# Kernel tuning notes

Hardware: AMD Instinct MI355X
Metric: run time of the kernel (lower is better)

Reference implementation:

```python
import jax, jax.numpy as jnp
import numpy as np

NHEAD = 8
LAYER_NAMES = ('self', 'cross', 'self', 'cross')
EPS = 1e-6


def ln(x, g, b, eps=1e-5):
    m = jnp.mean(x, -1, keepdims=True)
    v = jnp.mean((x - m) ** 2, -1, keepdims=True)
    return (x - m) * jax.lax.rsqrt(v + eps) * g + b


def linear_attention(q, k, v, q_mask, kv_mask):
    # q: [N, L, H, D], k/v: [N, S, H, D]; LoFTR LinearAttention (elu+1 feature map)
    Q = jax.nn.elu(q) + 1.0
    K = jax.nn.elu(k) + 1.0
    if q_mask is not None:
        Q = Q * q_mask[:, :, None, None].astype(Q.dtype)
    if kv_mask is not None:
        mk = kv_mask[:, :, None, None].astype(K.dtype)
        K = K * mk
        v = v * mk
    v_len = v.shape[1]
    v = v / v_len
    KV = jnp.einsum('nshd,nshv->nhdv', K, v)
    Z = 1.0 / (jnp.einsum('nlhd,nhd->nlh', Q, K.sum(1)) + EPS)
    return jnp.einsum('nlhd,nhdv,nlh->nlhv', Q, KV, Z) * v_len


def enc_layer(x, src, q_mask, kv_mask, Wq, Wk, Wv, Wm, W1, W2, g1, b1, g2, b2):
    # x: [N, L, C], src: [N, S, C]
    N, L, C = x.shape
    S = src.shape[1]
    H, D = NHEAD, C // NHEAD
    q = (x @ Wq).reshape(N, L, H, D)
    k = (src @ Wk).reshape(N, S, H, D)
    v = (src @ Wv).reshape(N, S, H, D)
    msg = linear_attention(q, k, v, q_mask, kv_mask).reshape(N, L, C)
    msg = ln(msg @ Wm, g1, b1)
    msg = ln(jnp.tanh(jnp.concatenate([x, msg], axis=-1) @ W1) @ W2, g2, b2)
    return x + msg


def sample_descriptors(kp, fmap, s):
    # kp: [B, L, K, 2] (x, y) raw-image pixel coords; fmap: [B, C, H, W]; s: stride
    B, C, H, W = fmap.shape
    k = kp - s / 2 + 0.5
    denom = jnp.array([W * s - s / 2 - 0.5, H * s - s / 2 - 0.5], dtype=kp.dtype)
    k = (k / denom) * 2.0 - 1.0  # normalized [-1, 1]
    px = (k[..., 0] + 1.0) * 0.5 * (W - 1)  # align_corners=True grid_sample
    py = (k[..., 1] + 1.0) * 0.5 * (H - 1)
    x0 = jnp.floor(px)
    y0 = jnp.floor(py)
    wx = (px - x0)[..., None]
    wy = (py - y0)[..., None]
    x0i = jnp.clip(x0, 0, W - 1).astype(jnp.int32)
    x1i = jnp.clip(x0 + 1, 0, W - 1).astype(jnp.int32)
    y0i = jnp.clip(y0, 0, H - 1).astype(jnp.int32)
    y1i = jnp.clip(y0 + 1, 0, H - 1).astype(jnp.int32)
    fm = jnp.transpose(fmap, (0, 2, 3, 1))  # [B, H, W, C]
    bidx = jnp.arange(B)[:, None, None]
    g00 = fm[bidx, y0i, x0i]
    g01 = fm[bidx, y0i, x1i]
    g10 = fm[bidx, y1i, x0i]
    g11 = fm[bidx, y1i, x1i]
    out = (1 - wy) * ((1 - wx) * g00 + wx * g01) + wy * ((1 - wx) * g10 + wx * g11)
    # SuperPoint-style L2 normalization of sampled descriptors
    out = out / (jnp.linalg.norm(out, axis=-1, keepdims=True) + 1e-8)
    return out  # [B, L, K, C]


def geo_transformer(feat0, feat1, kp0_cross, kp1_cross, mask_self0, mask_self1,
                    mask_cross0, mask_cross1, Wq, Wk, Wv, Wm, W1, W2, g1, b1, g2, b2,
                    h0, w0, h1, w1, scale):
    B, L0, C = feat0.shape
    L1 = feat1.shape[1]
    K = kp0_cross.shape[2]
    for i, name in enumerate(LAYER_NAMES):
        p = (Wq[i], Wk[i], Wv[i], Wm[i], W1[i], W2[i], g1[i], b1[i], g2[i], b2[i])
        if name == 'self':
            # source = masked subset of x == full source with kv-mask (v_length cancels)
            feat0 = enc_layer(feat0, feat0, None, mask_self0, *p)
            feat1 = enc_layer(feat1, feat1, None, mask_self1, *p)
        else:
            fmap0 = jnp.transpose(feat0.reshape(B, h0, w0, C), (0, 3, 1, 2))
            fmap1 = jnp.transpose(feat1.reshape(B, h1, w1, C), (0, 3, 1, 2))
            f0c = sample_descriptors(kp0_cross, fmap0, scale)  # [B, L1, K, C]
            f1c = sample_descriptors(kp1_cross, fmap1, scale)  # [B, L0, K, C]
            x0 = feat0.reshape(B * L0, 1, C)
            x1 = feat1.reshape(B * L1, 1, C)
            nf0 = enc_layer(x0, f1c.reshape(B * L0, K, C), None,
                            mask_cross1.reshape(B * L0, K), *p)
            nf1 = enc_layer(x1, f0c.reshape(B * L1, K, C), None,
                            mask_cross0.reshape(B * L1, K), *p)
            feat0 = nf0.reshape(B, L0, C)
            feat1 = nf1.reshape(B, L1, C)
    return feat0, feat1


def setup_inputs() -> dict:
    key = jax.random.key(0)
    B, H0, W0, C, K, S, NL = 2, 64, 64, 256, 9, 8, 4
    L = H0 * W0
    ks = jax.random.split(key, 16)
    std = (2.0 / (C + C)) ** 0.5
    std2 = (2.0 / (2 * C + 2 * C)) ** 0.5
    std3 = (2.0 / (2 * C + C)) ** 0.5
    kp0 = jnp.stack([
        jax.random.uniform(ks[2], (B, L, K)) * (W0 * S),
        jax.random.uniform(ks[3], (B, L, K)) * (H0 * S)], axis=-1)
    kp1 = jnp.stack([
        jax.random.uniform(ks[4], (B, L, K)) * (W0 * S),
        jax.random.uniform(ks[5], (B, L, K)) * (H0 * S)], axis=-1)
    return {
        'feat0': jax.random.normal(ks[0], (B, L, C), jnp.float32),
        'feat1': jax.random.normal(ks[1], (B, L, C), jnp.float32),
        'kp0_cross': kp0.astype(jnp.float32),
        'kp1_cross': kp1.astype(jnp.float32),
        'mask_self0': jax.random.bernoulli(ks[6], 0.9, (B, L)),
        'mask_self1': jax.random.bernoulli(ks[7], 0.9, (B, L)),
        'mask_cross0': jax.random.bernoulli(ks[8], 0.8, (B, L, K)),
        'mask_cross1': jax.random.bernoulli(ks[9], 0.8, (B, L, K)),
        'Wq': jax.random.normal(ks[10], (NL, C, C), jnp.float32) * std,
        'Wk': jax.random.normal(ks[11], (NL, C, C), jnp.float32) * std,
        'Wv': jax.random.normal(ks[12], (NL, C, C), jnp.float32) * std,
        'Wm': jax.random.normal(ks[13], (NL, C, C), jnp.float32) * std,
        'W1': jax.random.normal(ks[14], (NL, 2 * C, 2 * C), jnp.float32) * std2,
        'W2': jax.random.normal(ks[15], (NL, 2 * C, C), jnp.float32) * std3,
        'g1': jnp.ones((NL, C), jnp.float32),
        'b1': jnp.zeros((NL, C), jnp.float32),
        'g2': jnp.ones((NL, C), jnp.float32),
        'b2': jnp.zeros((NL, C), jnp.float32),
        'h0': H0, 'w0': W0, 'h1': H0, 'w1': W0, 'scale': S,
    }


def reference(feat0, feat1, kp0_cross, kp1_cross, mask_self0, mask_self1,
              mask_cross0, mask_cross1, Wq, Wk, Wv, Wm, W1, W2, g1, b1, g2, b2,
              h0, w0, h1, w1, scale):
    return geo_transformer(feat0, feat1, kp0_cross, kp1_cross, mask_self0, mask_self1,
                           mask_cross0, mask_cross1, Wq, Wk, Wv, Wm, W1, W2,
                           g1, b1, g2, b2, h0, w0, h1, w1, scale)
```

## Files before the change

### kernel.cpp

```cpp
#include <hip/hip_runtime.h>
#include <cstddef>


#define NROWS 16384

typedef unsigned short ushort_t;
typedef __attribute__((ext_vector_type(8))) short short8;
typedef __attribute__((ext_vector_type(4))) float f32x4;
typedef __attribute__((ext_vector_type(4))) unsigned short ushort4_t;
typedef __attribute__((ext_vector_type(8))) unsigned short ushort8_t;

__device__ __forceinline__ float b2f(unsigned short u) {
    union { unsigned int i; float f; } v; v.i = (unsigned int)u << 16; return v.f;
}
__device__ __forceinline__ unsigned short f2b(float x) {
    union { float f; unsigned int i; } v; v.f = x;
    unsigned int r = v.i + 0x7fffu + ((v.i >> 16) & 1u);
    return (unsigned short)(r >> 16);
}
__device__ __forceinline__ float elu1(float x) {
    return x > 0.f ? x + 1.f : __expf(x);
}

#define ASYNC_COPY16(gptr, lptr) \
    __builtin_amdgcn_global_load_lds((const __attribute__((address_space(1))) void*)(gptr), \
                                     (__attribute__((address_space(3))) void*)(lptr), 16, 0, 0)

template<int ACT>
__global__ __launch_bounds__(256) void gemm_bf16_kernel(
    const ushort_t* __restrict__ A0, const ushort_t* __restrict__ A1, int ksplit,
    int lda0, int lda1, const ushort_t* __restrict__ Wt, int ldw,
    ushort_t* __restrict__ C, int ldc, int Kd)
{
    __shared__ ushort_t As[128 * 32];
    __shared__ ushort_t Bs[128 * 32];

    int tid = threadIdx.x;
    int m0 = blockIdx.y * 128;
    int n0 = blockIdx.x * 128;
    int lane = tid & 63, w = tid >> 6;
    int wrow = w >> 1, wcol = w & 1;
    int quad = lane >> 4, l16 = lane & 15;

    f32x4 acc[4][4];
    #pragma unroll
    for (int i = 0; i < 4; i++)
        #pragma unroll
        for (int j = 0; j < 4; j++) acc[i][j] = (f32x4){0.f, 0.f, 0.f, 0.f};

    int c0 = tid, c1 = tid + 256;
    int ar0 = c0 >> 2, ac0 = (c0 & 3) * 8;
    int ar1 = c1 >> 2, ac1 = (c1 & 3) * 8;

    for (int kb = 0; kb < Kd; kb += 32) {
        const ushort_t* Ab; int lda, kc;
        if (kb < ksplit) { Ab = A0; lda = lda0; kc = kb; }
        else             { Ab = A1; lda = lda1; kc = kb - ksplit; }

        ASYNC_COPY16(Ab + (size_t)(m0 + ar0) * lda + kc + ac0, (char*)As + c0 * 16);
        ASYNC_COPY16(Ab + (size_t)(m0 + ar1) * lda + kc + ac1, (char*)As + c1 * 16);
        ASYNC_COPY16(Wt + (size_t)(n0 + ar0) * ldw + kb + ac0, (char*)Bs + c0 * 16);
        ASYNC_COPY16(Wt + (size_t)(n0 + ar1) * ldw + kb + ac1, (char*)Bs + c1 * 16);
        __syncthreads();

        short8 af[4], bf[4];
        #pragma unroll
        for (int mt = 0; mt < 4; mt++)
            af[mt] = *(const short8*)&As[(wrow * 64 + mt * 16 + l16) * 32 + quad * 8];
        #pragma unroll
        for (int nt = 0; nt < 4; nt++)
            bf[nt] = *(const short8*)&Bs[(wcol * 64 + nt * 16 + l16) * 32 + quad * 8];
        #pragma unroll
        for (int mt = 0; mt < 4; mt++)
            #pragma unroll
            for (int nt = 0; nt < 4; nt++)
                acc[mt][nt] = __builtin_amdgcn_mfma_f32_16x16x32_bf16(
                    af[mt], bf[nt], acc[mt][nt], 0, 0, 0);
        __syncthreads();
    }

    #pragma unroll
    for (int mt = 0; mt < 4; mt++) {
        int row = m0 + wrow * 64 + mt * 16 + quad * 4;
        #pragma unroll
        for (int nt = 0; nt < 4; nt++) {
            int col = n0 + wcol * 64 + nt * 16 + l16;
            #pragma unroll
            for (int r = 0; r < 4; r++) {
                float v = acc[mt][nt][r];
                if (ACT) v = tanhf(v);
                C[(size_t)(row + r) * ldc + col] = f2b(v);
            }
        }
    }
}

template<int RES>
__global__ __launch_bounds__(256) void gemm_ln_kernel(
    const ushort_t* __restrict__ A, int lda,
    const ushort_t* __restrict__ Wt, int ldw, int Kd,
    const float* __restrict__ g, const float* __restrict__ bp,
    ushort_t* __restrict__ OutBf,
    const float* __restrict__ Xin, float* __restrict__ Xout)
{
    __shared__ ushort_t As[64 * 64];
    __shared__ ushort_t Bs[256 * 64];
    __shared__ float rsum[4][64];
    __shared__ float rsq[4][64];

    int tid = threadIdx.x;
    int m0 = blockIdx.x * 64;
    int lane = tid & 63, w = tid >> 6;
    int quad = lane >> 4, l16 = lane & 15;

    f32x4 acc[4][4];
    #pragma unroll
    for (int i = 0; i < 4; i++)
        #pragma unroll
        for (int j = 0; j < 4; j++) acc[i][j] = (f32x4){0.f, 0.f, 0.f, 0.f};

    for (int kb = 0; kb < Kd; kb += 64) {
        #pragma unroll
        for (int q = 0; q < 2; q++) {
            int c = q * 256 + tid;
            ASYNC_COPY16(A + (size_t)(m0 + (c >> 3)) * lda + kb + (c & 7) * 8,
                         (char*)As + c * 16);
        }
        #pragma unroll
        for (int q = 0; q < 8; q++) {
            int c = q * 256 + tid;
            ASYNC_COPY16(Wt + (size_t)(c >> 3) * ldw + kb + (c & 7) * 8,
                         (char*)Bs + c * 16);
        }
        __syncthreads();

        #pragma unroll
        for (int kk = 0; kk < 2; kk++) {
            short8 af[4], bf[4];
            #pragma unroll
            for (int mt = 0; mt < 4; mt++)
                af[mt] = *(const short8*)&As[(mt * 16 + l16) * 64 + kk * 32 + quad * 8];
            #pragma unroll
            for (int nt = 0; nt < 4; nt++)
                bf[nt] = *(const short8*)&Bs[(w * 64 + nt * 16 + l16) * 64 + kk * 32 + quad * 8];
            #pragma unroll
            for (int mt = 0; mt < 4; mt++)
                #pragma unroll
                for (int nt = 0; nt < 4; nt++)
                    acc[mt][nt] = __builtin_amdgcn_mfma_f32_16x16x32_bf16(
                        af[mt], bf[nt], acc[mt][nt], 0, 0, 0);
        }
        __syncthreads();
    }

    float s1[4][4], s2[4][4];
    #pragma unroll
    for (int mt = 0; mt < 4; mt++)
        #pragma unroll
        for (int r = 0; r < 4; r++) {
            float s = 0.f, q = 0.f;
            #pragma unroll
            for (int nt = 0; nt < 4; nt++) {
                float v = acc[mt][nt][r];
                s += v; q += v * v;
            }
            #pragma unroll
            for (int off = 1; off < 16; off <<= 1) {
                s += __shfl_xor(s, off, 64);
                q += __shfl_xor(q, off, 64);
            }
            s1[mt][r] = s; s2[mt][r] = q;
        }
    if (l16 == 0) {
        #pragma unroll
        for (int mt = 0; mt < 4; mt++)
            #pragma unroll
            for (int r = 0; r < 4; r++) {
                rsum[w][mt * 16 + quad * 4 + r] = s1[mt][r];
                rsq[w][mt * 16 + quad * 4 + r]  = s2[mt][r];
            }
    }
    __syncthreads();

    #pragma unroll
    for (int mt = 0; mt < 4; mt++) {
        #pragma unroll
        for (int r = 0; r < 4; r++) {
            int rl = mt * 16 + quad * 4 + r;
            float s = rsum[0][rl] + rsum[1][rl] + rsum[2][rl] + rsum[3][rl];
            float q = rsq[0][rl] + rsq[1][rl] + rsq[2][rl] + rsq[3][rl];
            float m = s * (1.f / 256.f);
            float var = q * (1.f / 256.f) - m * m;
            float rs = rsqrtf(var + 1e-5f);
            size_t row = (size_t)(m0 + rl);
            #pragma unroll
            for (int nt = 0; nt < 4; nt++) {
                int col = w * 64 + nt * 16 + l16;
                float y = (acc[mt][nt][r] - m) * rs * g[col] + bp[col];
                if (RES) {
                    float xn = Xin[row * 256 + col] + y;
                    Xout[row * 256 + col] = xn;
                    OutBf[row * 256 + col] = f2b(xn);
                } else {
                    OutBf[row * 256 + col] = f2b(y);
                }
            }
        }
    }
}

__global__ __launch_bounds__(256) void wprep_kernel(
    const float* __restrict__ Wq, const float* __restrict__ Wk,
    const float* __restrict__ Wv, const float* __restrict__ Wm,
    const float* __restrict__ W1, const float* __restrict__ W2,
    ushort_t* __restrict__ Wqkvt, ushort_t* __restrict__ Wmt,
    ushort_t* __restrict__ W1t, ushort_t* __restrict__ W2t)
{
    int t = blockIdx.x;
    int layer = t / 640, r = t % 640;
    const float* src; ushort_t* dst;
    int ldsrc, lddst, tn, tk;
    if (r < 192) {
        int grp = r / 64, rr = r % 64; tn = rr / 8; tk = rr % 8;
        src = (grp == 0 ? Wq : grp == 1 ? Wk : Wv) + (size_t)layer * 65536;
        ldsrc = 256;
        dst = Wqkvt + (size_t)layer * 196608 + (size_t)grp * 65536;
        lddst = 256;
    } else if (r < 256) {
        int rr = r - 192; tn = rr / 8; tk = rr % 8;
        src = Wm + (size_t)layer * 65536; ldsrc = 256;
        dst = Wmt + (size_t)layer * 65536; lddst = 256;
    } else if (r < 512) {
        int rr = r - 256; tn = rr / 16; tk = rr % 16;
        src = W1 + (size_t)layer * 262144; ldsrc = 512;
        dst = W1t + (size_t)layer * 262144; lddst = 512;
    } else {
        int rr = r - 512; tn = rr / 16; tk = rr % 16;
        src = W2 + (size_t)layer * 131072; ldsrc = 256;
        dst = W2t + (size_t)layer * 131072; lddst = 512;
    }
    int n0 = tn * 32, k0 = tk * 32;
    __shared__ float tileS[32][33];
    int j = threadIdx.x & 31, i0 = threadIdx.x >> 5;
    #pragma unroll
    for (int p = 0; p < 4; p++) {
        int i = i0 + p * 8;
        tileS[i][j] = src[(size_t)(k0 + i) * ldsrc + n0 + j];
    }
    __syncthreads();
    #pragma unroll
    for (int p = 0; p < 4; p++) {
        int i = i0 + p * 8;
        dst[(size_t)(n0 + i) * lddst + k0 + j] = f2b(tileS[j][i]);
    }
}

__global__ __launch_bounds__(256) void init_kernel(
    const float* __restrict__ f0, const float* __restrict__ f1,
    float* __restrict__ X, ushort_t* __restrict__ Xbf)
{
    int idx = blockIdx.x * 256 + threadIdx.x;
    size_t e = (size_t)idx * 4;
    float4 v = (e < 2097152) ? *(const float4*)&f0[e] : *(const float4*)&f1[e - 2097152];
    *(float4*)&X[e] = v;
    ushort4_t u = { f2b(v.x), f2b(v.y), f2b(v.z), f2b(v.w) };
    *(ushort4_t*)&Xbf[e] = u;
}

__global__ __launch_bounds__(256) void kv_reduce_kernel(
    const ushort_t* __restrict__ QKV,
    const int* __restrict__ mask0, const int* __restrict__ mask1,
    float* __restrict__ KV, float* __restrict__ Ksum)
{
    int g = blockIdx.y;
    int t = g >> 4, b = (g >> 3) & 1, h = g & 7;
    const int* mask = t ? mask1 : mask0;
    int rowbase = t * 8192 + b * 4096;
    int s_begin = blockIdx.x * 256;

    __shared__ float sK[32][32];
    __shared__ float sV[32][32];

    int tid = threadIdx.x;
    int e  = tid & 31;
    int dq = tid >> 5;

    float acc[4] = {0.f, 0.f, 0.f, 0.f};
    float ks[4]  = {0.f, 0.f, 0.f, 0.f};

    for (int s0 = s_begin; s0 < s_begin + 256; s0 += 32) {
        #pragma unroll
        for (int q = 0; q < 2; q++) {
            int idx = tid + q * 256;
            int rl = idx >> 4;
            int part = idx & 15;
            int s = s0 + rl;
            size_t row = (size_t)(rowbase + s);
            float m = mask[b * 4096 + s] ? 1.f : 0.f;
            if (part < 8) {
                ushort4_t u = *(const ushort4_t*)&QKV[row * 768 + 256 + h * 32 + part * 4];
                float4 f = { elu1(b2f(u.x)) * m, elu1(b2f(u.y)) * m,
                             elu1(b2f(u.z)) * m, elu1(b2f(u.w)) * m };
                *(float4*)&sK[rl][part * 4] = f;
            } else {
                ushort4_t u = *(const ushort4_t*)&QKV[row * 768 + 512 + h * 32 + (part - 8) * 4];
                float4 f = { b2f(u.x) * m, b2f(u.y) * m, b2f(u.z) * m, b2f(u.w) * m };
                *(float4*)&sV[rl][(part - 8) * 4] = f;
            }
        }
        __syncthreads();

        #pragma unroll
        for (int s = 0; s < 32; s++) {
            float4 kq = *(const float4*)&sK[s][dq * 4];
            float vv = sV[s][e];
            acc[0] += kq.x * vv;
            acc[1] += kq.y * vv;
            acc[2] += kq.z * vv;
            acc[3] += kq.w * vv;
            ks[0] += kq.x; ks[1] += kq.y; ks[2] += kq.z; ks[3] += kq.w;
        }
        __syncthreads();
    }

    #pragma unroll
    for (int j = 0; j < 4; j++)
        atomicAdd(&KV[(size_t)g * 1024 + (dq * 4 + j) * 32 + e], acc[j]);
    if (e == 0) {
        #pragma unroll
        for (int j = 0; j < 4; j++)
            atomicAdd(&Ksum[g * 32 + dq * 4 + j], ks[j]);
    }
}

__global__ __launch_bounds__(256) void attn_apply_kernel(
    const ushort_t* __restrict__ QKV, const float* __restrict__ KV,
    const float* __restrict__ Ksum, ushort_t* __restrict__ MSG)
{
    int row = blockIdx.x;
    int t = row >> 13, bb = (row >> 12) & 1;
    int gb = (t * 2 + bb) * 8;
    int c = threadIdx.x, h = c >> 5, e = c & 31;
    int g = gb + h;

    __shared__ float sQ[256];
    float qf = elu1(b2f(QKV[(size_t)row * 768 + c]));
    sQ[c] = qf;
    __syncthreads();

    float p = qf * Ksum[g * 32 + e];
    #pragma unroll
    for (int off = 16; off; off >>= 1) p += __shfl_xor(p, off, 32);
    float Z = 1.f / (p + 1e-6f);

    float acc = 0.f;
    #pragma unroll
    for (int d = 0; d < 32; d++)
        acc += sQ[h * 32 + d] * KV[(size_t)g * 1024 + d * 32 + e];

    MSG[(size_t)row * 256 + c] = f2b(acc * Z);
}

__global__ __launch_bounds__(256) void gram_kernel(
    const ushort_t* __restrict__ Xbf, float* __restrict__ Gm)
{
    int a = blockIdx.x * 4 + (threadIdx.x >> 6);
    int lane = threadIdx.x & 63;
    int img = a / 4225;
    int rr = a - img * 4225;
    int ay = rr / 65, ax = rr - ay * 65;
    int xa = ax > 0 ? ax - 1 : 0;
    int xb = ax < 64 ? ax : 63;
    if (ax == 0) xb = 0;
    int ya = ay > 0 ? ay - 1 : 0;
    int yb = ay < 64 ? ay : 63;
    if (ay == 0) yb = 0;

    size_t rbase = (size_t)img * 4096;
    size_t r0 = (rbase + ya * 64 + xa) * 256;
    size_t r1 = (rbase + ya * 64 + xb) * 256;
    size_t r2 = (rbase + yb * 64 + xa) * 256;
    size_t r3 = (rbase + yb * 64 + xb) * 256;

    int c4 = lane * 4;
    ushort4_t u0 = *(const ushort4_t*)&Xbf[r0 + c4];
    ushort4_t u1 = *(const ushort4_t*)&Xbf[r1 + c4];
    ushort4_t u2 = *(const ushort4_t*)&Xbf[r2 + c4];
    ushort4_t u3 = *(const ushort4_t*)&Xbf[r3 + c4];

    float p[10] = {0,0,0,0,0,0,0,0,0,0};
    #pragma unroll
    for (int j = 0; j < 4; j++) {
        float f0 = b2f(u0[j]), f1 = b2f(u1[j]), f2 = b2f(u2[j]), f3 = b2f(u3[j]);
        p[0] += f0 * f0; p[1] += f0 * f1; p[2] += f0 * f2; p[3] += f0 * f3;
        p[4] += f1 * f1; p[5] += f1 * f2; p[6] += f1 * f3;
        p[7] += f2 * f2; p[8] += f2 * f3; p[9] += f3 * f3;
    }
    #pragma unroll
    for (int k = 0; k < 10; k++)
        #pragma unroll
        for (int off = 32; off; off >>= 1) p[k] += __shfl_xor(p[k], off, 64);

    if (lane == 0) {
        #pragma unroll
        for (int k = 0; k < 10; k++) Gm[(size_t)a * 10 + k] = p[k];
    }
}

__global__ __launch_bounds__(256) void cross_fused_kernel(
    const ushort_t* __restrict__ QKV, const float* __restrict__ Gm,
    const float* __restrict__ kp0, const float* __restrict__ kp1,
    const int* __restrict__ maskc0, const int* __restrict__ maskc1,
    ushort_t* __restrict__ MSG)
{
    int wv = threadIdx.x >> 6;
    int lane = threadIdx.x & 63;
    int half = lane >> 5;
    int l32 = lane & 31;
    int row = blockIdx.x * 8 + wv * 2 + half;

    int t = row >> 13;
    int bl = row & 8191;
    int ts = 1 - t;
    const float* kp = ts ? kp1 : kp0;
    const int* mask = (t == 0) ? maskc1 : maskc0;
    int img = ts * 2 + (bl >> 12);
    size_t rb = (size_t)img * 4096;
    const float* Gimg = Gm + (size_t)img * 42250;

    int c8 = l32 * 8;

    ushort8_t qu = *(const ushort8_t*)&QKV[(size_t)row * 768 + c8];
    float qf[8];
    #pragma unroll
    for (int j = 0; j < 8; j++) qf[j] = elu1(b2f(qu[j]));

    float zsum = 0.f;
    float acc[8] = {0,0,0,0,0,0,0,0};

    for (int s9 = 0; s9 < 9; s9++) {
        int r = bl * 9 + s9;
        bool mk = mask[r] != 0;
        if (mk) {
            float xx = kp[(size_t)r * 2 + 0];
            float yy = kp[(size_t)r * 2 + 1];
            float px = (xx - 3.5f) * (63.f / 507.5f);
            float py = (yy - 3.5f) * (63.f / 507.5f);
            float fx = floorf(px), fy = floorf(py);
            float wx = px - fx, wy = py - fy;
            int ix = (int)fx, iy = (int)fy;
            int xa = ix > 0 ? ix : 0;
            int xb = ix + 1 > 0 ? (ix + 1 < 63 ? ix + 1 : 63) : 0;
            int ya = iy > 0 ? iy : 0;
            int yb = iy + 1 > 0 ? (iy + 1 < 63 ? iy + 1 : 63) : 0;

            float w0 = (1.f - wy) * (1.f - wx);
            float w1 = (1.f - wy) * wx;
            float w2 = wy * (1.f - wx);
            float w3 = wy * wx;

            const float* G = &Gimg[(size_t)((iy + 1) * 65 + (ix + 1)) * 10];
            float g00 = G[0], g01 = G[1], g02 = G[2], g03 = G[3], g11 = G[4];
            float g12 = G[5], g13 = G[6], g22 = G[7], g23 = G[8], g33 = G[9];
            float ss = w0 * w0 * g00 + w1 * w1 * g11 + w2 * w2 * g22 + w3 * w3 * g33
                     + 2.f * (w0 * w1 * g01 + w0 * w2 * g02 + w0 * w3 * g03
                            + w1 * w2 * g12 + w1 * w3 * g13 + w2 * w3 * g23);
            float inv = 1.f / (sqrtf(ss) + 1e-8f);
            float u0 = w0 * inv, u1 = w1 * inv, u2 = w2 * inv, u3 = w3 * inv;

            size_t s00 = (rb + ya * 64 + xa) * 768;
            size_t s01 = (rb + ya * 64 + xb) * 768;
            size_t s10 = (rb + yb * 64 + xa) * 768;
            size_t s11 = (rb + yb * 64 + xb) * 768;

            ushort8_t k00 = *(const ushort8_t*)&QKV[s00 + 256 + c8];
            ushort8_t k01 = *(const ushort8_t*)&QKV[s01 + 256 + c8];
            ushort8_t k10 = *(const ushort8_t*)&QKV[s10 + 256 + c8];
            ushort8_t k11 = *(const ushort8_t*)&QKV[s11 + 256 + c8];
            ushort8_t v00 = *(const ushort8_t*)&QKV[s00 + 512 + c8];
            ushort8_t v01 = *(const ushort8_t*)&QKV[s01 + 512 + c8];
            ushort8_t v10 = *(const ushort8_t*)&QKV[s10 + 512 + c8];
            ushort8_t v11 = *(const ushort8_t*)&QKV[s11 + 512 + c8];

            float vc[8];
            float p = 0.f;
            #pragma unroll
            for (int j = 0; j < 8; j++) {
                float kc = u0 * b2f(k00[j]) + u1 * b2f(k01[j])
                         + u2 * b2f(k10[j]) + u3 * b2f(k11[j]);
                vc[j] = u0 * b2f(v00[j]) + u1 * b2f(v01[j])
                      + u2 * b2f(v10[j]) + u3 * b2f(v11[j]);
                p += qf[j] * elu1(kc);
            }
            p += __shfl_xor(p, 1, 64);
            p += __shfl_xor(p, 2, 64);

            zsum += p;
            #pragma unroll
            for (int j = 0; j < 8; j++) acc[j] += p * vc[j];
        }
    }

    float Z = 1.f / (zsum + 1e-6f);
    ushort8_t o;
    #pragma unroll
    for (int j = 0; j < 8; j++) o[j] = f2b(acc[j] * Z);
    *(ushort8_t*)&MSG[(size_t)row * 256 + c8] = o;
}


extern "C" void kernel_launch(void* const* d_in, const int* in_sizes, int n_in,
                              void* d_out, int out_size, void* d_ws, size_t ws_size,
                              hipStream_t stream)
{
    const float* feat0 = (const float*)d_in[0];
    const float* feat1 = (const float*)d_in[1];
    const float* kp0 = (const float*)d_in[2];
    const float* kp1 = (const float*)d_in[3];
    const int* ms0 = (const int*)d_in[4];
    const int* ms1 = (const int*)d_in[5];
    const int* mc0 = (const int*)d_in[6];
    const int* mc1 = (const int*)d_in[7];
    const float* Wq = (const float*)d_in[8];
    const float* Wk = (const float*)d_in[9];
    const float* Wv = (const float*)d_in[10];
    const float* Wm = (const float*)d_in[11];
    const float* W1 = (const float*)d_in[12];
    const float* W2 = (const float*)d_in[13];
    const float* g1 = (const float*)d_in[14];
    const float* b1 = (const float*)d_in[15];
    const float* g2 = (const float*)d_in[16];
    const float* b2 = (const float*)d_in[17];

    char* p = (char*)d_ws;
    float*    X     = (float*)p;            p += 16777216;
    ushort_t* Xbf   = (ushort_t*)p;         p += 8388608;
    ushort_t* QKV   = (ushort_t*)p;         p += 25165824;
    ushort_t* MSG   = (ushort_t*)p;         p += 8388608;
    ushort_t* T     = (ushort_t*)p;         p += 16777216;
    ushort_t* L1bf  = (ushort_t*)p;         p += 8388608;
    float*    KVb   = (float*)p;            p += 131072;
    float*    KSb   = (float*)p;            p += 4096;
    float*    Gm    = (float*)p;            p += 679936;
    ushort_t* Wqkvt = (ushort_t*)p;         p += 1572864;
    ushort_t* Wmt   = (ushort_t*)p;         p += 524288;
    ushort_t* W1t   = (ushort_t*)p;         p += 2097152;
    ushort_t* W2t   = (ushort_t*)p;         p += 1048576;

    init_kernel<<<4096, 256, 0, stream>>>(feat0, feat1, X, Xbf);
    wprep_kernel<<<2560, 256, 0, stream>>>(Wq, Wk, Wv, Wm, W1, W2, Wqkvt, Wmt, W1t, W2t);

    auto gemm = [&](const ushort_t* A0, const ushort_t* A1, int ksplit, int lda0, int lda1,
                    const ushort_t* Wtp, int ldw, ushort_t* Cp, int ldc, int N, int Kd, int act) {
        dim3 grid(N / 128, NROWS / 128);
        if (act)
            gemm_bf16_kernel<1><<<grid, 256, 0, stream>>>(A0, A1, ksplit, lda0, lda1, Wtp, ldw, Cp, ldc, Kd);
        else
            gemm_bf16_kernel<0><<<grid, 256, 0, stream>>>(A0, A1, ksplit, lda0, lda1, Wtp, ldw, Cp, ldc, Kd);
    };

    for (int i = 0; i < 4; i++) {
        const ushort_t* Wqkvt_l = Wqkvt + (size_t)i * 196608;
        const ushort_t* Wmt_l   = Wmt   + (size_t)i * 65536;
        const ushort_t* W1t_l   = W1t   + (size_t)i * 262144;
        const ushort_t* W2t_l   = W2t   + (size_t)i * 131072;
        const float* g1_l = g1 + (size_t)i * 256;
        const float* b1_l = b1 + (size_t)i * 256;
        const float* g2_l = g2 + (size_t)i * 256;
        const float* b2_l = b2 + (size_t)i * 256;
        bool is_self = (i == 0 || i == 2);

        gemm(Xbf, nullptr, 1 << 30, 256, 0, Wqkvt_l, 256, QKV, 768, 768, 256, 0);

        if (is_self) {
            hipMemsetAsync(KVb, 0, 33792 * 4, stream);
            kv_reduce_kernel<<<dim3(16, 32), 256, 0, stream>>>(QKV, ms0, ms1, KVb, KSb);
            attn_apply_kernel<<<NROWS, 256, 0, stream>>>(QKV, KVb, KSb, MSG);
        } else {
            gram_kernel<<<4225, 256, 0, stream>>>(Xbf, Gm);
            cross_fused_kernel<<<NROWS / 8, 256, 0, stream>>>(QKV, Gm, kp0, kp1, mc0, mc1, MSG);
        }

        gemm_ln_kernel<0><<<NROWS / 64, 256, 0, stream>>>(
            MSG, 256, Wmt_l, 256, 256, g1_l, b1_l, L1bf, nullptr, nullptr);
        gemm(Xbf, L1bf, 256, 256, 256, W1t_l, 512, T, 512, 512, 512, 1);
        float* Xout = (i == 3) ? (float*)d_out : X;
        gemm_ln_kernel<1><<<NROWS / 64, 256, 0, stream>>>(
            T, 512, W2t_l, 512, 512, g2_l, b2_l, Xbf, X, Xout);
    }
}
```

Before: 653.2 us.

## Deepen GEMM K-tile, halve LN-GEMM row tile, split cross-attn samples across half-waves

The generic bf16 GEMM now stages a K=64 slab per iteration, stored as two 32-wide subtiles in LDS, which halves the barrier count per K. The fused GEMM+LayerNorm kernel drops to 32-row tiles to launch twice as many blocks, and its LDS layout is repacked into 32-wide K subtiles. The cross-attention kernel gives each wave a single row, splits the 9 keypoint samples between the two half-waves, and merges the partial sums with a cross-lane shuffle. Together these aim for more parallelism and fewer syncs, at the cost of more LDS per GEMM block and reloading the full weight tile for each smaller LN block.

Result: faster. 638.6 us (-2.2%).

```diff
diff --git a/kernel.cpp b/kernel.cpp
--- a/kernel.cpp
+++ b/kernel.cpp
@@ -32,8 +32,8 @@
     int lda0, int lda1, const ushort_t* __restrict__ Wt, int ldw,
     ushort_t* __restrict__ C, int ldc, int Kd)
 {
-    __shared__ ushort_t As[128 * 32];
-    __shared__ ushort_t Bs[128 * 32];
+    __shared__ ushort_t As[128 * 64];
+    __shared__ ushort_t Bs[128 * 64];
 
     int tid = threadIdx.x;
     int m0 = blockIdx.y * 128;
@@ -48,34 +48,45 @@
         #pragma unroll
         for (int j = 0; j < 4; j++) acc[i][j] = (f32x4){0.f, 0.f, 0.f, 0.f};
 
-    int c0 = tid, c1 = tid + 256;
-    int ar0 = c0 >> 2, ac0 = (c0 & 3) * 8;
-    int ar1 = c1 >> 2, ac1 = (c1 & 3) * 8;
-
-    for (int kb = 0; kb < Kd; kb += 32) {
+    for (int kb = 0; kb < Kd; kb += 64) {
         const ushort_t* Ab; int lda, kc;
         if (kb < ksplit) { Ab = A0; lda = lda0; kc = kb; }
         else             { Ab = A1; lda = lda1; kc = kb - ksplit; }
 
-        ASYNC_COPY16(Ab + (size_t)(m0 + ar0) * lda + kc + ac0, (char*)As + c0 * 16);
-        ASYNC_COPY16(Ab + (size_t)(m0 + ar1) * lda + kc + ac1, (char*)As + c1 * 16);
-        ASYNC_COPY16(Wt + (size_t)(n0 + ar0) * ldw + kb + ac0, (char*)Bs + c0 * 16);
-        ASYNC_COPY16(Wt + (size_t)(n0 + ar1) * ldw + kb + ac1, (char*)Bs + c1 * 16);
+        #pragma unroll
+        for (int q = 0; q < 4; q++) {
+            int s = q * 256 + tid;
+            int kk = s >> 9, p = s & 511;
+            int row = p >> 2, c4 = p & 3;
+            ASYNC_COPY16(Ab + (size_t)(m0 + row) * lda + kc + kk * 32 + c4 * 8,
+                         (char*)As + s * 16);
+        }
+        #pragma unroll
+        for (int q = 0; q < 4; q++) {
+            int s = q * 256 + tid;
+            int kk = s >> 9, p = s & 511;
+            int row = p >> 2, c4 = p & 3;
+            ASYNC_COPY16(Wt + (size_t)(n0 + row) * ldw + kb + kk * 32 + c4 * 8,
+                         (char*)Bs + s * 16);
+        }
         __syncthreads();
 
-        short8 af[4], bf[4];
-        #pragma unroll
-        for (int mt = 0; mt < 4; mt++)
-            af[mt] = *(const short8*)&As[(wrow * 64 + mt * 16 + l16) * 32 + quad * 8];
-        #pragma unroll
-        for (int nt = 0; nt < 4; nt++)
-            bf[nt] = *(const short8*)&Bs[(wcol * 64 + nt * 16 + l16) * 32 + quad * 8];
-        #pragma unroll
-        for (int mt = 0; mt < 4; mt++)
+        #pragma unroll
+        for (int kk = 0; kk < 2; kk++) {
+            short8 af[4], bf[4];
+            #pragma unroll
+            for (int mt = 0; mt < 4; mt++)
+                af[mt] = *(const short8*)&As[kk * 4096 + (wrow * 64 + mt * 16 + l16) * 32 + quad * 8];
             #pragma unroll
             for (int nt = 0; nt < 4; nt++)
-                acc[mt][nt] = __builtin_amdgcn_mfma_f32_16x16x32_bf16(
-                    af[mt], bf[nt], acc[mt][nt], 0, 0, 0);
+                bf[nt] = *(const short8*)&Bs[kk * 4096 + (wcol * 64 + nt * 16 + l16) * 32 + quad * 8];
+            #pragma unroll
+            for (int mt = 0; mt < 4; mt++)
+                #pragma unroll
+                for (int nt = 0; nt < 4; nt++)
+                    acc[mt][nt] = __builtin_amdgcn_mfma_f32_16x16x32_bf16(
+                        af[mt], bf[nt], acc[mt][nt], 0, 0, 0);
+        }
         __syncthreads();
     }
 
@@ -103,48 +114,51 @@
     ushort_t* __restrict__ OutBf,
     const float* __restrict__ Xin, float* __restrict__ Xout)
 {
-    __shared__ ushort_t As[64 * 64];
+    __shared__ ushort_t As[32 * 64];
     __shared__ ushort_t Bs[256 * 64];
-    __shared__ float rsum[4][64];
-    __shared__ float rsq[4][64];
+    __shared__ float rsum[4][32];
+    __shared__ float rsq[4][32];
 
     int tid = threadIdx.x;
-    int m0 = blockIdx.x * 64;
+    int m0 = blockIdx.x * 32;
     int lane = tid & 63, w = tid >> 6;
     int quad = lane >> 4, l16 = lane & 15;
 
-    f32x4 acc[4][4];
-    #pragma unroll
-    for (int i = 0; i < 4; i++)
+    f32x4 acc[2][4];
+    #pragma unroll
+    for (int i = 0; i < 2; i++)
         #pragma unroll
         for (int j = 0; j < 4; j++) acc[i][j] = (f32x4){0.f, 0.f, 0.f, 0.f};
 
     for (int kb = 0; kb < Kd; kb += 64) {
-        #pragma unroll
-        for (int q = 0; q < 2; q++) {
-            int c = q * 256 + tid;
-            ASYNC_COPY16(A + (size_t)(m0 + (c >> 3)) * lda + kb + (c & 7) * 8,
-                         (char*)As + c * 16);
+        {
+            int s = tid;
+            int kk = s >> 7, p = s & 127;
+            int row = p >> 2, c4 = p & 3;
+            ASYNC_COPY16(A + (size_t)(m0 + row) * lda + kb + kk * 32 + c4 * 8,
+                         (char*)As + s * 16);
         }
         #pragma unroll
         for (int q = 0; q < 8; q++) {
-            int c = q * 256 + tid;
-            ASYNC_COPY16(Wt + (size_t)(c >> 3) * ldw + kb + (c & 7) * 8,
-                         (char*)Bs + c * 16);
+            int s = q * 256 + tid;
+            int kk = s >> 10, p = s & 1023;
+            int row = p >> 2, c4 = p & 3;
+            ASYNC_COPY16(Wt + (size_t)(row) * ldw + kb + kk * 32 + c4 * 8,
+                         (char*)Bs + s * 16);
         }
         __syncthreads();
 
         #pragma unroll
         for (int kk = 0; kk < 2; kk++) {
-            short8 af[4], bf[4];
-            #pragma unroll
-            for (int mt = 0; mt < 4; mt++)
-                af[mt] = *(const short8*)&As[(mt * 16 + l16) * 64 + kk * 32 + quad * 8];
+            short8 af[2], bf[4];
+            #pragma unroll
+            for (int mt = 0; mt < 2; mt++)
+                af[mt] = *(const short8*)&As[kk * 1024 + (mt * 16 + l16) * 32 + quad * 8];
             #pragma unroll
             for (int nt = 0; nt < 4; nt++)
-                bf[nt] = *(const short8*)&Bs[(w * 64 + nt * 16 + l16) * 64 + kk * 32 + quad * 8];
-            #pragma unroll
-            for (int mt = 0; mt < 4; mt++)
+                bf[nt] = *(const short8*)&Bs[kk * 8192 + (w * 64 + nt * 16 + l16) * 32 + quad * 8];
+            #pragma unroll
+            for (int mt = 0; mt < 2; mt++)
                 #pragma unroll
                 for (int nt = 0; nt < 4; nt++)
                     acc[mt][nt] = __builtin_amdgcn_mfma_f32_16x16x32_bf16(
@@ -153,9 +167,8 @@
         __syncthreads();
     }
 
-    float s1[4][4], s2[4][4];
-    #pragma unroll
-    for (int mt = 0; mt < 4; mt++)
+    #pragma unroll
+    for (int mt = 0; mt < 2; mt++)
         #pragma unroll
         for (int r = 0; r < 4; r++) {
             float s = 0.f, q = 0.f;
@@ -169,21 +182,15 @@
                 s += __shfl_xor(s, off, 64);
                 q += __shfl_xor(q, off, 64);
             }
-            s1[mt][r] = s; s2[mt][r] = q;
-        }
-    if (l16 == 0) {
-        #pragma unroll
-        for (int mt = 0; mt < 4; mt++)
-            #pragma unroll
-            for (int r = 0; r < 4; r++) {
-                rsum[w][mt * 16 + quad * 4 + r] = s1[mt][r];
-                rsq[w][mt * 16 + quad * 4 + r]  = s2[mt][r];
+            if (l16 == 0) {
+                rsum[w][mt * 16 + quad * 4 + r] = s;
+                rsq[w][mt * 16 + quad * 4 + r]  = q;
             }
-    }
+        }
     __syncthreads();
 
     #pragma unroll
-    for (int mt = 0; mt < 4; mt++) {
+    for (int mt = 0; mt < 2; mt++) {
         #pragma unroll
         for (int r = 0; r < 4; r++) {
             int rl = mt * 16 + quad * 4 + r;
@@ -417,7 +424,7 @@
     int lane = threadIdx.x & 63;
     int half = lane >> 5;
     int l32 = lane & 31;
-    int row = blockIdx.x * 8 + wv * 2 + half;
+    int row = blockIdx.x * 4 + wv;
 
     int t = row >> 13;
     int bl = row & 8191;
@@ -438,7 +445,7 @@
     float zsum = 0.f;
     float acc[8] = {0,0,0,0,0,0,0,0};
 
-    for (int s9 = 0; s9 < 9; s9++) {
+    for (int s9 = half; s9 < 9; s9 += 2) {
         int r = bl * 9 + s9;
         bool mk = mask[r] != 0;
         if (mk) {
@@ -501,11 +508,17 @@
         }
     }
 
-    float Z = 1.f / (zsum + 1e-6f);
-    ushort8_t o;
-    #pragma unroll
-    for (int j = 0; j < 8; j++) o[j] = f2b(acc[j] * Z);
-    *(ushort8_t*)&MSG[(size_t)row * 256 + c8] = o;
+    zsum += __shfl_xor(zsum, 32, 64);
+    #pragma unroll
+    for (int j = 0; j < 8; j++) acc[j] += __shfl_xor(acc[j], 32, 64);
+
+    if (half == 0) {
+        float Z = 1.f / (zsum + 1e-6f);
+        ushort8_t o;
+        #pragma unroll
+        for (int j = 0; j < 8; j++) o[j] = f2b(acc[j] * Z);
+        *(ushort8_t*)&MSG[(size_t)row * 256 + c8] = o;
+    }
 }
 
 
@@ -578,14 +591,14 @@
             attn_apply_kernel<<<NROWS, 256, 0, stream>>>(QKV, KVb, KSb, MSG);
         } else {
             gram_kernel<<<4225, 256, 0, stream>>>(Xbf, Gm);
-            cross_fused_kernel<<<NROWS / 8, 256, 0, stream>>>(QKV, Gm, kp0, kp1, mc0, mc1, MSG);
-        }
-
-        gemm_ln_kernel<0><<<NROWS / 64, 256, 0, stream>>>(
+            cross_fused_kernel<<<NROWS / 4, 256, 0, stream>>>(QKV, Gm, kp0, kp1, mc0, mc1, MSG);
+        }
+
+        gemm_ln_kernel<0><<<NROWS / 32, 256, 0, stream>>>(
             MSG, 256, Wmt_l, 256, 256, g1_l, b1_l, L1bf, nullptr, nullptr);
         gemm(Xbf, L1bf, 256, 256, 256, W1t_l, 512, T, 512, 512, 512, 1);
         float* Xout = (i == 3) ? (float*)d_out : X;
-        gemm_ln_kernel<1><<<NROWS / 64, 256, 0, stream>>>(
+        gemm_ln_kernel<1><<<NROWS / 32, 256, 0, stream>>>(
             T, 512, W2t_l, 512, 512, g2_l, b2_l, Xbf, X, Xout);
     }
 }
```
